# Optimization experiments

Hardware: AMD Instinct MI355X
Metric: run time of the kernel (lower is better)

## Reference

```python
import jax, jax.numpy as jnp
import numpy as np

N_NODES = 50000
N_EDGES = 800000
IN_DIM = 64
HID = 64
OUT_DIM = 40
NEG_SLOPE = 0.2


def _gat_layer(x, src, dst, W, b, att, bias, n_nodes):
    # x: [N, Fin] -> lin -> [N, Fout]; heads = 1
    h = x @ W.T + b
    x_i = h[dst]                      # [E, F] target features
    x_j = h[src]                      # [E, F] source features
    # edge attention logits: cat([x_i, x_j]) @ att.T -> [E, 1]
    alpha = jnp.concatenate([x_i, x_j], axis=-1) @ att.T
    alpha = jax.nn.leaky_relu(alpha, NEG_SLOPE)
    # segment softmax over destination node (pyg_utils.softmax)
    amax = jax.ops.segment_max(alpha, dst, num_segments=n_nodes)
    e = jnp.exp(alpha - amax[dst])
    denom = jax.ops.segment_sum(e, dst, num_segments=n_nodes)
    alpha = e / (denom[dst] + 1e-16)
    # message = alpha * x_j, aggr='add' scatter to dst, then + bias
    out = jax.ops.segment_sum(x_j * alpha, dst, num_segments=n_nodes)
    return out + bias


def setup_inputs() -> dict:
    key = jax.random.key(0)
    ks = jax.random.split(key, 12)
    x = jax.random.normal(ks[0], (N_NODES, IN_DIM), dtype=jnp.float32)
    edge_index = jax.random.randint(ks[1], (2, N_EDGES), 0, N_NODES, dtype=jnp.int64)
    def glorot(k, shape):
        fan_in, fan_out = shape[1], shape[0]
        lim = float(np.sqrt(6.0 / (fan_in + fan_out)))
        return jax.random.uniform(k, shape, jnp.float32, -lim, lim)
    W1 = glorot(ks[2], (HID, IN_DIM))
    b1 = jnp.zeros((HID,), jnp.float32)
    att1 = glorot(ks[3], (1, 2 * HID))
    bias1 = jnp.zeros((HID,), jnp.float32)
    W2 = glorot(ks[4], (HID, HID))
    b2 = jnp.zeros((HID,), jnp.float32)
    att2 = glorot(ks[5], (1, 2 * HID))
    bias2 = jnp.zeros((HID,), jnp.float32)
    Wp1 = glorot(ks[6], (HID, HID))
    bp1 = jnp.zeros((HID,), jnp.float32)
    Wp2 = glorot(ks[7], (OUT_DIM, HID))
    bp2 = jnp.zeros((OUT_DIM,), jnp.float32)
    return {"x": x, "edge_index": edge_index,
            "W1": W1, "b1": b1, "att1": att1, "bias1": bias1,
            "W2": W2, "b2": b2, "att2": att2, "bias2": bias2,
            "Wp1": Wp1, "bp1": bp1, "Wp2": Wp2, "bp2": bp2}


def reference(x, edge_index, W1, b1, att1, bias1, W2, b2, att2, bias2,
              Wp1, bp1, Wp2, bp2):
    src, dst = edge_index[0], edge_index[1]
    n = x.shape[0]
    # layer 1 (GAT) + relu; dropout p=0 in eval -> identity
    h = jax.nn.relu(_gat_layer(x, src, dst, W1, b1, att1, bias1, n))
    # layer 2 (GAT) + relu
    h = jax.nn.relu(_gat_layer(h, src, dst, W2, b2, att2, bias2, n))
    # post-MP MLP + log_softmax over classes
    h = h @ Wp1.T + bp1
    logits = h @ Wp2.T + bp2
    return jax.nn.log_softmax(logits, axis=1)
```

## Files before the change

### kernel.cpp

```cpp
#include <hip/hip_runtime.h>
#include <hip/hip_fp16.h>
#include <math.h>

#define NN 50000
#define NE 800000
#define NEG 0.2f

#define NPB 128
#define CHK 6250
#define NBUK 98
#define LCAP 10240

typedef __attribute__((ext_vector_type(8))) short short8v;
typedef __attribute__((ext_vector_type(4))) float f32x4;

__device__ __forceinline__ float lrelu(float x){ return x > 0.f ? x : NEG * x; }

__device__ __forceinline__ float bcastf(float v, int l){
    return __uint_as_float(__builtin_amdgcn_readlane(__float_as_uint(v), l));
}
__device__ __forceinline__ short bf16t(float x){ return (short)(__float_as_uint(x) >> 16); }
__device__ __forceinline__ float bf16tof(short s){
    return __uint_as_float(((unsigned)(unsigned short)s) << 16);
}

__global__ __launch_bounds__(256) void k_cntA(const int* __restrict__ dst,
                                              int* __restrict__ counts){
    __shared__ int c[NBUK];
    int tid = threadIdx.x, blk = blockIdx.x;
    for (int i = tid; i < NBUK; i += 256) c[i] = 0;
    __syncthreads();
    int beg = blk * CHK, end = min(beg + CHK, NE);
    for (int i = beg + tid; i < end; i += 256) atomicAdd(&c[dst[i] >> 9], 1);
    __syncthreads();
    for (int i = tid; i < NBUK; i += 256) counts[i * NPB + blk] = c[i];
}

__global__ __launch_bounds__(1024) void k_scanB(int* __restrict__ counts,
                                                int* __restrict__ bbase){
    __shared__ int swave[16];
    int tid = threadIdx.x, lane = tid & 63, wid = tid >> 6;
    const int M = NBUK * NPB;
    int carry = 0;
    for (int base = 0; base < M; base += 1024){
        int i = base + tid;
        int v = (i < M) ? counts[i] : 0;
        int incl = v;
        #pragma unroll
        for (int off = 1; off < 64; off <<= 1){
            int t = __shfl_up(incl, off);
            if (lane >= off) incl += t;
        }
        if (lane == 63) swave[wid] = incl;
        __syncthreads();
        if (wid == 0){
            int sv = (lane < 16) ? swave[lane] : 0;
            #pragma unroll
            for (int off = 1; off < 16; off <<= 1){
                int t = __shfl_up(sv, off);
                if (lane >= off) sv += t;
            }
            if (lane < 16) swave[lane] = sv;
        }
        __syncthreads();
        int woff = wid ? swave[wid - 1] : 0;
        if (i < M) counts[i] = carry + woff + incl - v;
        carry += swave[15];
        __syncthreads();
    }
    for (int i = tid; i < NBUK; i += 1024) bbase[i] = counts[i * NPB];
    if (tid == 0) bbase[NBUK] = NE;
}

__global__ __launch_bounds__(256) void k_partC(const int* __restrict__ src,
                                               const int* __restrict__ dst,
                                               const int* __restrict__ cofs,
                                               unsigned* __restrict__ part){
    __shared__ int lcur[NBUK];
    int tid = threadIdx.x, blk = blockIdx.x;
    for (int i = tid; i < NBUK; i += 256) lcur[i] = cofs[i * NPB + blk];
    __syncthreads();
    int beg = blk * CHK, end = min(beg + CHK, NE);
    for (int i = beg + tid; i < end; i += 256){
        int d = dst[i];
        int pos = atomicAdd(&lcur[d >> 9], 1);
        part[pos] = ((unsigned)(d & 511) << 16) | (unsigned)src[i];
    }
}

__global__ __launch_bounds__(256) void k_buildD(const unsigned* __restrict__ part,
                                                const int* __restrict__ bbase,
                                                int* __restrict__ rowstart,
                                                int* __restrict__ csr){
    __shared__ int hist[512], cur[512];
    __shared__ int csrbuf[LCAP];
    __shared__ int swave[4];
    int tid = threadIdx.x, lane = tid & 63, wid = tid >> 6;
    int b = blockIdx.x;
    int ebeg = bbase[b], eend = bbase[b + 1], cnt = eend - ebeg;

    for (int i = tid; i < 512; i += 256) hist[i] = 0;
    __syncthreads();
    for (int i = tid; i < cnt; i += 256) atomicAdd(&hist[part[ebeg + i] >> 16], 1);
    __syncthreads();

    int h0 = hist[2 * tid], h1 = hist[2 * tid + 1];
    int v = h0 + h1, incl = v;
    #pragma unroll
    for (int off = 1; off < 64; off <<= 1){
        int t = __shfl_up(incl, off);
        if (lane >= off) incl += t;
    }
    if (lane == 63) swave[wid] = incl;
    __syncthreads();
    int woff = 0;
    #pragma unroll
    for (int w = 0; w < 4; ++w) if (w < wid) woff += swave[w];
    int e0 = woff + incl - v;
    int e1 = e0 + h0;
    cur[2 * tid] = e0; cur[2 * tid + 1] = e1;
    int gi = b * 512 + 2 * tid;
    if (gi     <= NN) rowstart[gi]     = ebeg + e0;
    if (gi + 1 <= NN) rowstart[gi + 1] = ebeg + e1;
    __syncthreads();

    for (int i = tid; i < cnt; i += 256){
        unsigned u = part[ebeg + i];
        int lp = atomicAdd(&cur[u >> 16], 1);
        if (lp < LCAP) csrbuf[lp] = (int)(u & 0xFFFFu);
    }
    __syncthreads();
    int m = min(cnt, LCAP);
    for (int i = tid; i < m; i += 256) csr[ebeg + i] = csrbuf[i];
}

__global__ __launch_bounds__(256) void k_prep(const float* __restrict__ W1,
                                              const float* __restrict__ W2,
                                              const float* __restrict__ Wp1,
                                              const float* __restrict__ bp1,
                                              const float* __restrict__ Wp2,
                                              const float* __restrict__ bp2,
                                              short8v* __restrict__ w1h, short8v* __restrict__ w1l,
                                              short8v* __restrict__ w2h, short8v* __restrict__ w2l,
                                              short8v* __restrict__ wch, short8v* __restrict__ wcl,
                                              float* __restrict__ bc){
    int tid = threadIdx.x, b = blockIdx.x;
    if (b < 2){
        const float* W = b ? W2 : W1;
        short8v* Wh = b ? w2h : w1h;
        short8v* Wl = b ? w2l : w1l;
        for (int p = tid; p < 512; p += 256){
            int f = p >> 6, lane = p & 63;
            int nt = f >> 1, ks = f & 1;
            int r0 = lane & 15, rg = lane >> 4;
            const float* wp = W + (size_t)(nt * 16 + r0) * 64 + ks * 32 + rg * 8;
            short8v hi, lo;
            #pragma unroll
            for (int j = 0; j < 8; ++j){
                float v = wp[j];
                short h = bf16t(v);
                hi[j] = h; lo[j] = bf16t(v - bf16tof(h));
            }
            Wh[p] = hi; Wl[p] = lo;
        }
    } else {
        __shared__ float wc[2560];
        for (int i = tid; i < 2560; i += 256){
            int c = i >> 6, k = i & 63;
            float s = 0.f;
            #pragma unroll 8
            for (int j = 0; j < 64; ++j) s = fmaf(Wp2[c * 64 + j], Wp1[j * 64 + k], s);
            wc[i] = s;
        }
        if (tid < 40){
            float s = bp2[tid];
            for (int j = 0; j < 64; ++j) s = fmaf(Wp2[tid * 64 + j], bp1[j], s);
            bc[tid] = s;
        }
        __syncthreads();
        for (int p = tid; p < 384; p += 256){
            int f = p >> 6, lane = p & 63;
            int nt = f >> 1, ks = f & 1;
            int r0 = lane & 15, rg = lane >> 4;
            int fr = nt * 16 + r0; if (fr > 39) fr = 39;
            short8v hi, lo;
            #pragma unroll
            for (int j = 0; j < 8; ++j){
                float v = wc[fr * 64 + ks * 32 + rg * 8 + j];
                short h = bf16t(v);
                hi[j] = h; lo[j] = bf16t(v - bf16tof(h));
            }
            wch[p] = hi; wcl[p] = lo;
        }
    }
}

__global__ __launch_bounds__(256) void k_lin_mfma(const float* __restrict__ X,
                                                  const short8v* __restrict__ Wh,
                                                  const short8v* __restrict__ Wl,
                                                  const float* __restrict__ b,
                                                  const float* __restrict__ att,
                                                  __half* __restrict__ Hh,
                                                  float* __restrict__ ad,
                                                  float* __restrict__ as_, int n){
    int lane = threadIdx.x & 63, wid = threadIdx.x >> 6;
    int nb = blockIdx.x * 64 + wid * 16;
    if (nb >= n) return;
    int r0 = lane & 15, rg = lane >> 4;

    short8v a_hi[2], a_lo[2];
    int arow = nb + r0; if (arow >= n) arow = n - 1;
    const float* xp = X + (size_t)arow * 64 + rg * 8;
    #pragma unroll
    for (int ks = 0; ks < 2; ++ks){
        #pragma unroll
        for (int j = 0; j < 8; ++j){
            float v = xp[ks * 32 + j];
            short h = bf16t(v);
            a_hi[ks][j] = h;
            a_lo[ks][j] = bf16t(v - bf16tof(h));
        }
    }

    f32x4 acc[4] = {{0,0,0,0},{0,0,0,0},{0,0,0,0},{0,0,0,0}};
    #pragma unroll
    for (int nt = 0; nt < 4; ++nt){
        #pragma unroll
        for (int ks = 0; ks < 2; ++ks){
            short8v b_hi = Wh[(nt * 2 + ks) * 64 + lane];
            short8v b_lo = Wl[(nt * 2 + ks) * 64 + lane];
            acc[nt] = __builtin_amdgcn_mfma_f32_16x16x32_bf16(a_hi[ks], b_hi, acc[nt], 0, 0, 0);
            acc[nt] = __builtin_amdgcn_mfma_f32_16x16x32_bf16(a_hi[ks], b_lo, acc[nt], 0, 0, 0);
            acc[nt] = __builtin_amdgcn_mfma_f32_16x16x32_bf16(a_lo[ks], b_hi, acc[nt], 0, 0, 0);
        }
    }

    #pragma unroll
    for (int nt = 0; nt < 4; ++nt){
        float bb = b[nt * 16 + r0];
        #pragma unroll
        for (int q = 0; q < 4; ++q){
            int node = nb + rg * 4 + q;
            float v = acc[nt][q] + bb;
            acc[nt][q] = v;
            if (node < n) Hh[(size_t)node * 64 + nt * 16 + r0] = __float2half(v);
        }
    }

    float attd[4], atts[4];
    #pragma unroll
    for (int nt = 0; nt < 4; ++nt){
        attd[nt] = att[nt * 16 + r0];
        atts[nt] = att[64 + nt * 16 + r0];
    }
    #pragma unroll
    for (int q = 0; q < 4; ++q){
        float pd = 0.f, ps = 0.f;
        #pragma unroll
        for (int nt = 0; nt < 4; ++nt){
            pd = fmaf(attd[nt], acc[nt][q], pd);
            ps = fmaf(atts[nt], acc[nt][q], ps);
        }
        #pragma unroll
        for (int off = 8; off; off >>= 1){
            pd += __shfl_xor(pd, off);
            ps += __shfl_xor(ps, off);
        }
        int node = nb + rg * 4 + q;
        if (r0 == 0 && node < n){ ad[node] = pd; as_[node] = ps; }
    }
}

__global__ __launch_bounds__(256) void k_agg(const __half2* __restrict__ H2,
                                             const float* __restrict__ ad,
                                             const float* __restrict__ as_,
                                             const int* __restrict__ rowstart,
                                             const int* __restrict__ csr,
                                             const float2* __restrict__ bias2,
                                             float2* __restrict__ OUT2, int n){
    int tid = threadIdx.x, lane = tid & 63, wid = tid >> 6;
    int node = blockIdx.x * 4 + wid;
    if (node >= n) return;
    int beg = rowstart[node], end = rowstart[node + 1];
    float adn = ad[node];
    int half = lane >> 5, hl = lane & 31;

    float accx = 0.f, accy = 0.f, denom = 0.f;
    for (int cbeg = beg; cbeg < end; cbeg += 64){
        int k = cbeg + lane;
        int s = (k < end) ? csr[k] : 0;
        float e = (k < end) ? __expf(lrelu(adn + as_[s])) : 0.f;
        float es = e;
        #pragma unroll
        for (int off = 32; off; off >>= 1) es += __shfl_xor(es, off);
        denom += es;
        int cnt = min(64, end - cbeg);
        int j = 0;
        for (; j + 4 <= cnt; j += 4){
            int i0 = j + half, i1 = j + 2 + half;
            int   s0 = __shfl(s, i0), s1 = __shfl(s, i1);
            float e0 = __shfl(e, i0), e1 = __shfl(e, i1);
            __half2 ha = H2[(size_t)s0 * 32 + hl];
            __half2 hb = H2[(size_t)s1 * 32 + hl];
            float2 fa = __half22float2(ha), fb = __half22float2(hb);
            accx = fmaf(e0, fa.x, accx); accy = fmaf(e0, fa.y, accy);
            accx = fmaf(e1, fb.x, accx); accy = fmaf(e1, fb.y, accy);
        }
        for (; j < cnt; j += 2){
            int idx = j + half;
            int   se = __shfl(s, idx);
            float ee = __shfl(e, idx);
            float2 f = __half22float2(H2[(size_t)se * 32 + hl]);
            accx = fmaf(ee, f.x, accx); accy = fmaf(ee, f.y, accy);
        }
    }
    accx += __shfl_xor(accx, 32);
    accy += __shfl_xor(accy, 32);
    if (half == 0){
        float2 bb = bias2[hl];
        float inv = 1.f / (denom + 1e-16f);
        float2 o;
        o.x = fmaxf(fmaf(accx, inv, bb.x), 0.f);
        o.y = fmaxf(fmaf(accy, inv, bb.y), 0.f);
        OUT2[(size_t)node * 32 + hl] = o;
    }
}

__global__ __launch_bounds__(256) void k_mlp_mfma(const float* __restrict__ G,
                                                  const short8v* __restrict__ Wh,
                                                  const short8v* __restrict__ Wl,
                                                  const float* __restrict__ bc,
                                                  float* __restrict__ out, int n){
    int lane = threadIdx.x & 63, wid = threadIdx.x >> 6;
    int nb = blockIdx.x * 64 + wid * 16;
    if (nb >= n) return;
    int r0 = lane & 15, rg = lane >> 4;

    short8v a_hi[2], a_lo[2];
    int arow = nb + r0; if (arow >= n) arow = n - 1;
    const float* gp = G + (size_t)arow * 64 + rg * 8;
    #pragma unroll
    for (int ks = 0; ks < 2; ++ks){
        #pragma unroll
        for (int j = 0; j < 8; ++j){
            float v = gp[ks * 32 + j];
            short h = bf16t(v);
            a_hi[ks][j] = h;
            a_lo[ks][j] = bf16t(v - bf16tof(h));
        }
    }

    f32x4 acc[3] = {{0,0,0,0},{0,0,0,0},{0,0,0,0}};
    #pragma unroll
    for (int nt = 0; nt < 3; ++nt){
        #pragma unroll
        for (int ks = 0; ks < 2; ++ks){
            short8v b_hi = Wh[(nt * 2 + ks) * 64 + lane];
            short8v b_lo = Wl[(nt * 2 + ks) * 64 + lane];
            acc[nt] = __builtin_amdgcn_mfma_f32_16x16x32_bf16(a_hi[ks], b_hi, acc[nt], 0, 0, 0);
            acc[nt] = __builtin_amdgcn_mfma_f32_16x16x32_bf16(a_hi[ks], b_lo, acc[nt], 0, 0, 0);
            acc[nt] = __builtin_amdgcn_mfma_f32_16x16x32_bf16(a_lo[ks], b_hi, acc[nt], 0, 0, 0);
        }
    }

    float bcv[3];
    #pragma unroll
    for (int nt = 0; nt < 3; ++nt){
        int f = nt * 16 + r0;
        bcv[nt] = (f < 40) ? bc[f] : 0.f;
    }

    #pragma unroll
    for (int q = 0; q < 4; ++q){
        int node = nb + rg * 4 + q;
        float l0 = acc[0][q] + bcv[0];
        float l1 = acc[1][q] + bcv[1];
        float l2 = (32 + r0 < 40) ? acc[2][q] + bcv[2] : -INFINITY;
        float m = fmaxf(l0, fmaxf(l1, l2));
        #pragma unroll
        for (int off = 8; off; off >>= 1) m = fmaxf(m, __shfl_xor(m, off));
        float s = __expf(l0 - m) + __expf(l1 - m) + ((32 + r0 < 40) ? __expf(l2 - m) : 0.f);
        #pragma unroll
        for (int off = 8; off; off >>= 1) s += __shfl_xor(s, off);
        float lse = m + __logf(s);
        if (node < n){
            out[(size_t)node * 40 + r0]      = l0 - lse;
            out[(size_t)node * 40 + 16 + r0] = l1 - lse;
            if (32 + r0 < 40) out[(size_t)node * 40 + 32 + r0] = l2 - lse;
        }
    }
}

extern "C" void kernel_launch(void* const* d_in, const int* in_sizes, int n_in,
                              void* d_out, int out_size, void* d_ws, size_t ws_size,
                              hipStream_t stream){
    const float* x     = (const float*)d_in[0];
    const int*   ei    = (const int*)  d_in[1];
    const float* W1    = (const float*)d_in[2];
    const float* b1    = (const float*)d_in[3];
    const float* att1  = (const float*)d_in[4];
    const float* bias1 = (const float*)d_in[5];
    const float* W2    = (const float*)d_in[6];
    const float* b2    = (const float*)d_in[7];
    const float* att2  = (const float*)d_in[8];
    const float* bias2 = (const float*)d_in[9];
    const float* Wp1   = (const float*)d_in[10];
    const float* bp1   = (const float*)d_in[11];
    const float* Wp2   = (const float*)d_in[12];
    const float* bp2   = (const float*)d_in[13];
    float* out = (float*)d_out;

    float*    base     = (float*)d_ws;
    float*    g        = base;
    __half*   hh       = (__half*)(base + 3200000);
    unsigned* part     = (unsigned*)(base + 4800000);
    int*      csr      = (int*)(base + 5600000);
    int*      counts   = (int*)(base + 6400000);
    int*      bbase    = (int*)(base + 6412800);
    int*      rowstart = (int*)(base + 6413000);
    float*    ad       = base + 6463008;
    float*    as_      = base + 6513008;
    float*    bc       = base + 6563008;
    short8v*  w1h      = (short8v*)(base + 6563072);
    short8v*  w1l      = (short8v*)(base + 6565120);
    short8v*  w2h      = (short8v*)(base + 6567168);
    short8v*  w2l      = (short8v*)(base + 6569216);
    short8v*  wch      = (short8v*)(base + 6571264);
    short8v*  wcl      = (short8v*)(base + 6572800);

    const int* srcv = ei;
    const int* dstv = ei + NE;

    k_cntA  <<<NPB, 256, 0, stream>>>(dstv, counts);
    k_prep  <<<3, 256, 0, stream>>>(W1, W2, Wp1, bp1, Wp2, bp2,
                                    w1h, w1l, w2h, w2l, wch, wcl, bc);
    k_scanB <<<1, 1024, 0, stream>>>(counts, bbase);
    k_partC <<<NPB, 256, 0, stream>>>(srcv, dstv, counts, part);
    k_buildD<<<NBUK, 256, 0, stream>>>(part, bbase, rowstart, csr);

    int gb = (NN + 63) / 64;
    int nb = (NN + 3) / 4;
    k_lin_mfma<<<gb, 256, 0, stream>>>(x, w1h, w1l, b1, att1, hh, ad, as_, NN);
    k_agg     <<<nb, 256, 0, stream>>>((const __half2*)hh, ad, as_, rowstart, csr,
                                       (const float2*)bias1, (float2*)g, NN);
    k_lin_mfma<<<gb, 256, 0, stream>>>(g, w2h, w2l, b2, att2, hh, ad, as_, NN);
    k_agg     <<<nb, 256, 0, stream>>>((const __half2*)hh, ad, as_, rowstart, csr,
                                       (const float2*)bias2, (float2*)g, NN);
    k_mlp_mfma<<<gb, 256, 0, stream>>>(g, wch, wcl, bc, out, NN);
}
```

Measured before the change: 163.3 us.

## Fuse layer-1 linear, edge counting and MLP weight prep into one launch

Merges the first GAT linear transform, the dst-bucket histogram and the combined MLP weight computation into one heterogeneous kernel launch. The single-block serial scan is replaced by a two-stage parallel scan. Weight bf16 hi/lo splitting now happens inline in the MFMA kernels, which removes the separate prep kernel. The aggregation inner loop is also unrolled to issue four gathers at a time. Together these cut launch count and serialization in the CSR-build phase, at the cost of redundant per-block weight conversion and an extra small scan launch.

```diff
diff --git a/kernel.cpp b/kernel.cpp
--- a/kernel.cpp
+++ b/kernel.cpp
@@ -10,6 +10,7 @@
 #define CHK 6250
 #define NBUK 98
 #define LCAP 10240
+#define GB 782
 
 typedef __attribute__((ext_vector_type(8))) short short8v;
 typedef __attribute__((ext_vector_type(4))) float f32x4;
@@ -24,61 +25,176 @@
     return __uint_as_float(((unsigned)(unsigned short)s) << 16);
 }
 
-__global__ __launch_bounds__(256) void k_cntA(const int* __restrict__ dst,
-                                              int* __restrict__ counts){
+__device__ __forceinline__ void lin_body(int blk, int tid,
+                                         const float* __restrict__ X,
+                                         const float* __restrict__ W,
+                                         const float* __restrict__ b,
+                                         const float* __restrict__ att,
+                                         __half* __restrict__ Hh,
+                                         float* __restrict__ ad,
+                                         float* __restrict__ as_, int n){
+    int lane = tid & 63, wid = tid >> 6;
+    int nb = blk * 64 + wid * 16;
+    if (nb >= n) return;
+    int r0 = lane & 15, rg = lane >> 4;
+
+    short8v a_hi[2], a_lo[2];
+    int arow = nb + r0; if (arow >= n) arow = n - 1;
+    const float* xp = X + (size_t)arow * 64 + rg * 8;
+    #pragma unroll
+    for (int ks = 0; ks < 2; ++ks){
+        #pragma unroll
+        for (int j = 0; j < 8; ++j){
+            float v = xp[ks * 32 + j];
+            short h = bf16t(v);
+            a_hi[ks][j] = h;
+            a_lo[ks][j] = bf16t(v - bf16tof(h));
+        }
+    }
+
+    f32x4 acc[4] = {{0,0,0,0},{0,0,0,0},{0,0,0,0},{0,0,0,0}};
+    #pragma unroll
+    for (int nt = 0; nt < 4; ++nt){
+        const float* wp = W + (size_t)(nt * 16 + r0) * 64 + rg * 8;
+        #pragma unroll
+        for (int ks = 0; ks < 2; ++ks){
+            short8v b_hi, b_lo;
+            #pragma unroll
+            for (int j = 0; j < 8; ++j){
+                float v = wp[ks * 32 + j];
+                short h = bf16t(v);
+                b_hi[j] = h;
+                b_lo[j] = bf16t(v - bf16tof(h));
+            }
+            acc[nt] = __builtin_amdgcn_mfma_f32_16x16x32_bf16(a_hi[ks], b_hi, acc[nt], 0, 0, 0);
+            acc[nt] = __builtin_amdgcn_mfma_f32_16x16x32_bf16(a_hi[ks], b_lo, acc[nt], 0, 0, 0);
+            acc[nt] = __builtin_amdgcn_mfma_f32_16x16x32_bf16(a_lo[ks], b_hi, acc[nt], 0, 0, 0);
+        }
+    }
+
+    #pragma unroll
+    for (int nt = 0; nt < 4; ++nt){
+        float bb = b[nt * 16 + r0];
+        #pragma unroll
+        for (int q = 0; q < 4; ++q){
+            int node = nb + rg * 4 + q;
+            float v = acc[nt][q] + bb;
+            acc[nt][q] = v;
+            if (node < n) Hh[(size_t)node * 64 + nt * 16 + r0] = __float2half(v);
+        }
+    }
+
+    float attd[4], atts[4];
+    #pragma unroll
+    for (int nt = 0; nt < 4; ++nt){
+        attd[nt] = att[nt * 16 + r0];
+        atts[nt] = att[64 + nt * 16 + r0];
+    }
+    #pragma unroll
+    for (int q = 0; q < 4; ++q){
+        float pd = 0.f, ps = 0.f;
+        #pragma unroll
+        for (int nt = 0; nt < 4; ++nt){
+            pd = fmaf(attd[nt], acc[nt][q], pd);
+            ps = fmaf(atts[nt], acc[nt][q], ps);
+        }
+        #pragma unroll
+        for (int off = 8; off; off >>= 1){
+            pd += __shfl_xor(pd, off);
+            ps += __shfl_xor(ps, off);
+        }
+        int node = nb + rg * 4 + q;
+        if (r0 == 0 && node < n){ ad[node] = pd; as_[node] = ps; }
+    }
+}
+
+__global__ __launch_bounds__(256) void k_fuse0(const float* __restrict__ X,
+                                               const float* __restrict__ W1,
+                                               const float* __restrict__ b1,
+                                               const float* __restrict__ att1,
+                                               __half* __restrict__ Hh,
+                                               float* __restrict__ ad,
+                                               float* __restrict__ as_,
+                                               const int* __restrict__ dst,
+                                               int* __restrict__ counts,
+                                               const float* __restrict__ Wp1,
+                                               const float* __restrict__ bp1,
+                                               const float* __restrict__ Wp2,
+                                               const float* __restrict__ bp2,
+                                               float* __restrict__ Wc,
+                                               float* __restrict__ bc){
     __shared__ int c[NBUK];
     int tid = threadIdx.x, blk = blockIdx.x;
-    for (int i = tid; i < NBUK; i += 256) c[i] = 0;
-    __syncthreads();
-    int beg = blk * CHK, end = min(beg + CHK, NE);
-    for (int i = beg + tid; i < end; i += 256) atomicAdd(&c[dst[i] >> 9], 1);
-    __syncthreads();
-    for (int i = tid; i < NBUK; i += 256) counts[i * NPB + blk] = c[i];
-}
-
-__global__ __launch_bounds__(1024) void k_scanB(int* __restrict__ counts,
-                                                int* __restrict__ bbase){
-    __shared__ int swave[16];
+    if (blk < GB){
+        lin_body(blk, tid, X, W1, b1, att1, Hh, ad, as_, NN);
+    } else if (blk < GB + NPB){
+        int cb = blk - GB;
+        for (int i = tid; i < NBUK; i += 256) c[i] = 0;
+        __syncthreads();
+        int beg = cb * CHK, end = min(beg + CHK, NE);
+        for (int i = beg + tid; i < end; i += 256) atomicAdd(&c[dst[i] >> 9], 1);
+        __syncthreads();
+        for (int i = tid; i < NBUK; i += 256) counts[i * NPB + cb] = c[i];
+    } else {
+        for (int idx = tid; idx < 2560; idx += 256){
+            int cc = idx >> 6, k = idx & 63;
+            float s = 0.f;
+            #pragma unroll 8
+            for (int j = 0; j < 64; ++j) s = fmaf(Wp2[cc * 64 + j], Wp1[j * 64 + k], s);
+            Wc[idx] = s;
+        }
+        if (tid < 40){
+            float s = bp2[tid];
+            for (int j = 0; j < 64; ++j) s = fmaf(Wp2[tid * 64 + j], bp1[j], s);
+            bc[tid] = s;
+        }
+    }
+}
+
+__global__ __launch_bounds__(NPB) void k_scan1(int* __restrict__ counts,
+                                               int* __restrict__ tot){
+    __shared__ int wsum[2];
+    int b = blockIdx.x, tid = threadIdx.x, lane = tid & 63, wid = tid >> 6;
+    int v = counts[b * NPB + tid];
+    int incl = v;
+    #pragma unroll
+    for (int off = 1; off < 64; off <<= 1){
+        int t = __shfl_up(incl, off);
+        if (lane >= off) incl += t;
+    }
+    if (lane == 63) wsum[wid] = incl;
+    __syncthreads();
+    int excl = incl - v + (wid ? wsum[0] : 0);
+    counts[b * NPB + tid] = excl;
+    if (tid == NPB - 1) tot[b] = excl + v;
+}
+
+__global__ __launch_bounds__(128) void k_scan2(const int* __restrict__ tot,
+                                               int* __restrict__ bbase){
+    __shared__ int wsum[2];
     int tid = threadIdx.x, lane = tid & 63, wid = tid >> 6;
-    const int M = NBUK * NPB;
-    int carry = 0;
-    for (int base = 0; base < M; base += 1024){
-        int i = base + tid;
-        int v = (i < M) ? counts[i] : 0;
-        int incl = v;
-        #pragma unroll
-        for (int off = 1; off < 64; off <<= 1){
-            int t = __shfl_up(incl, off);
-            if (lane >= off) incl += t;
-        }
-        if (lane == 63) swave[wid] = incl;
-        __syncthreads();
-        if (wid == 0){
-            int sv = (lane < 16) ? swave[lane] : 0;
-            #pragma unroll
-            for (int off = 1; off < 16; off <<= 1){
-                int t = __shfl_up(sv, off);
-                if (lane >= off) sv += t;
-            }
-            if (lane < 16) swave[lane] = sv;
-        }
-        __syncthreads();
-        int woff = wid ? swave[wid - 1] : 0;
-        if (i < M) counts[i] = carry + woff + incl - v;
-        carry += swave[15];
-        __syncthreads();
-    }
-    for (int i = tid; i < NBUK; i += 1024) bbase[i] = counts[i * NPB];
-    if (tid == 0) bbase[NBUK] = NE;
+    int v = (tid < NBUK) ? tot[tid] : 0;
+    int incl = v;
+    #pragma unroll
+    for (int off = 1; off < 64; off <<= 1){
+        int t = __shfl_up(incl, off);
+        if (lane >= off) incl += t;
+    }
+    if (lane == 63) wsum[wid] = incl;
+    __syncthreads();
+    int excl = incl - v + (wid ? wsum[0] : 0);
+    if (tid < NBUK) bbase[tid] = excl;
+    if (tid == NBUK - 1) bbase[NBUK] = excl + v;
 }
 
 __global__ __launch_bounds__(256) void k_partC(const int* __restrict__ src,
                                                const int* __restrict__ dst,
                                                const int* __restrict__ cofs,
+                                               const int* __restrict__ bbase,
                                                unsigned* __restrict__ part){
     __shared__ int lcur[NBUK];
     int tid = threadIdx.x, blk = blockIdx.x;
-    for (int i = tid; i < NBUK; i += 256) lcur[i] = cofs[i * NPB + blk];
+    for (int i = tid; i < NBUK; i += 256) lcur[i] = bbase[i] + cofs[i * NPB + blk];
     __syncthreads();
     int beg = blk * CHK, end = min(beg + CHK, NE);
     for (int i = beg + tid; i < end; i += 256){
@@ -134,141 +250,14 @@
     for (int i = tid; i < m; i += 256) csr[ebeg + i] = csrbuf[i];
 }
 
-__global__ __launch_bounds__(256) void k_prep(const float* __restrict__ W1,
-                                              const float* __restrict__ W2,
-                                              const float* __restrict__ Wp1,
-                                              const float* __restrict__ bp1,
-                                              const float* __restrict__ Wp2,
-                                              const float* __restrict__ bp2,
-                                              short8v* __restrict__ w1h, short8v* __restrict__ w1l,
-                                              short8v* __restrict__ w2h, short8v* __restrict__ w2l,
-                                              short8v* __restrict__ wch, short8v* __restrict__ wcl,
-                                              float* __restrict__ bc){
-    int tid = threadIdx.x, b = blockIdx.x;
-    if (b < 2){
-        const float* W = b ? W2 : W1;
-        short8v* Wh = b ? w2h : w1h;
-        short8v* Wl = b ? w2l : w1l;
-        for (int p = tid; p < 512; p += 256){
-            int f = p >> 6, lane = p & 63;
-            int nt = f >> 1, ks = f & 1;
-            int r0 = lane & 15, rg = lane >> 4;
-            const float* wp = W + (size_t)(nt * 16 + r0) * 64 + ks * 32 + rg * 8;
-            short8v hi, lo;
-            #pragma unroll
-            for (int j = 0; j < 8; ++j){
-                float v = wp[j];
-                short h = bf16t(v);
-                hi[j] = h; lo[j] = bf16t(v - bf16tof(h));
-            }
-            Wh[p] = hi; Wl[p] = lo;
-        }
-    } else {
-        __shared__ float wc[2560];
-        for (int i = tid; i < 2560; i += 256){
-            int c = i >> 6, k = i & 63;
-            float s = 0.f;
-            #pragma unroll 8
-            for (int j = 0; j < 64; ++j) s = fmaf(Wp2[c * 64 + j], Wp1[j * 64 + k], s);
-            wc[i] = s;
-        }
-        if (tid < 40){
-            float s = bp2[tid];
-            for (int j = 0; j < 64; ++j) s = fmaf(Wp2[tid * 64 + j], bp1[j], s);
-            bc[tid] = s;
-        }
-        __syncthreads();
-        for (int p = tid; p < 384; p += 256){
-            int f = p >> 6, lane = p & 63;
-            int nt = f >> 1, ks = f & 1;
-            int r0 = lane & 15, rg = lane >> 4;
-            int fr = nt * 16 + r0; if (fr > 39) fr = 39;
-            short8v hi, lo;
-            #pragma unroll
-            for (int j = 0; j < 8; ++j){
-                float v = wc[fr * 64 + ks * 32 + rg * 8 + j];
-                short h = bf16t(v);
-                hi[j] = h; lo[j] = bf16t(v - bf16tof(h));
-            }
-            wch[p] = hi; wcl[p] = lo;
-        }
-    }
-}
-
 __global__ __launch_bounds__(256) void k_lin_mfma(const float* __restrict__ X,
-                                                  const short8v* __restrict__ Wh,
-                                                  const short8v* __restrict__ Wl,
+                                                  const float* __restrict__ W,
                                                   const float* __restrict__ b,
                                                   const float* __restrict__ att,
                                                   __half* __restrict__ Hh,
                                                   float* __restrict__ ad,
                                                   float* __restrict__ as_, int n){
-    int lane = threadIdx.x & 63, wid = threadIdx.x >> 6;
-    int nb = blockIdx.x * 64 + wid * 16;
-    if (nb >= n) return;
-    int r0 = lane & 15, rg = lane >> 4;
-
-    short8v a_hi[2], a_lo[2];
-    int arow = nb + r0; if (arow >= n) arow = n - 1;
-    const float* xp = X + (size_t)arow * 64 + rg * 8;
-    #pragma unroll
-    for (int ks = 0; ks < 2; ++ks){
-        #pragma unroll
-        for (int j = 0; j < 8; ++j){
-            float v = xp[ks * 32 + j];
-            short h = bf16t(v);
-            a_hi[ks][j] = h;
-            a_lo[ks][j] = bf16t(v - bf16tof(h));
-        }
-    }
-
-    f32x4 acc[4] = {{0,0,0,0},{0,0,0,0},{0,0,0,0},{0,0,0,0}};
-    #pragma unroll
-    for (int nt = 0; nt < 4; ++nt){
-        #pragma unroll
-        for (int ks = 0; ks < 2; ++ks){
-            short8v b_hi = Wh[(nt * 2 + ks) * 64 + lane];
-            short8v b_lo = Wl[(nt * 2 + ks) * 64 + lane];
-            acc[nt] = __builtin_amdgcn_mfma_f32_16x16x32_bf16(a_hi[ks], b_hi, acc[nt], 0, 0, 0);
-            acc[nt] = __builtin_amdgcn_mfma_f32_16x16x32_bf16(a_hi[ks], b_lo, acc[nt], 0, 0, 0);
-            acc[nt] = __builtin_amdgcn_mfma_f32_16x16x32_bf16(a_lo[ks], b_hi, acc[nt], 0, 0, 0);
-        }
-    }
-
-    #pragma unroll
-    for (int nt = 0; nt < 4; ++nt){
-        float bb = b[nt * 16 + r0];
-        #pragma unroll
-        for (int q = 0; q < 4; ++q){
-            int node = nb + rg * 4 + q;
-            float v = acc[nt][q] + bb;
-            acc[nt][q] = v;
-            if (node < n) Hh[(size_t)node * 64 + nt * 16 + r0] = __float2half(v);
-        }
-    }
-
-    float attd[4], atts[4];
-    #pragma unroll
-    for (int nt = 0; nt < 4; ++nt){
-        attd[nt] = att[nt * 16 + r0];
-        atts[nt] = att[64 + nt * 16 + r0];
-    }
-    #pragma unroll
-    for (int q = 0; q < 4; ++q){
-        float pd = 0.f, ps = 0.f;
-        #pragma unroll
-        for (int nt = 0; nt < 4; ++nt){
-            pd = fmaf(attd[nt], acc[nt][q], pd);
-            ps = fmaf(atts[nt], acc[nt][q], ps);
-        }
-        #pragma unroll
-        for (int off = 8; off; off >>= 1){
-            pd += __shfl_xor(pd, off);
-            ps += __shfl_xor(ps, off);
-        }
-        int node = nb + rg * 4 + q;
-        if (r0 == 0 && node < n){ ad[node] = pd; as_[node] = ps; }
-    }
+    lin_body(blockIdx.x, threadIdx.x, X, W, b, att, Hh, ad, as_, n);
 }
 
 __global__ __launch_bounds__(256) void k_agg(const __half2* __restrict__ H2,
@@ -296,13 +285,27 @@
         denom += es;
         int cnt = min(64, end - cbeg);
         int j = 0;
+        for (; j + 8 <= cnt; j += 8){
+            int i0 = j + half, i1 = j + 2 + half, i2 = j + 4 + half, i3 = j + 6 + half;
+            int   s0 = __shfl(s, i0), s1 = __shfl(s, i1), s2 = __shfl(s, i2), s3 = __shfl(s, i3);
+            float e0 = __shfl(e, i0), e1 = __shfl(e, i1), e2 = __shfl(e, i2), e3 = __shfl(e, i3);
+            __half2 ha = H2[(size_t)s0 * 32 + hl];
+            __half2 hb = H2[(size_t)s1 * 32 + hl];
+            __half2 hc = H2[(size_t)s2 * 32 + hl];
+            __half2 hd = H2[(size_t)s3 * 32 + hl];
+            float2 fa = __half22float2(ha), fb = __half22float2(hb);
+            float2 fc = __half22float2(hc), fd = __half22float2(hd);
+            accx = fmaf(e0, fa.x, accx); accy = fmaf(e0, fa.y, accy);
+            accx = fmaf(e1, fb.x, accx); accy = fmaf(e1, fb.y, accy);
+            accx = fmaf(e2, fc.x, accx); accy = fmaf(e2, fc.y, accy);
+            accx = fmaf(e3, fd.x, accx); accy = fmaf(e3, fd.y, accy);
+        }
         for (; j + 4 <= cnt; j += 4){
             int i0 = j + half, i1 = j + 2 + half;
             int   s0 = __shfl(s, i0), s1 = __shfl(s, i1);
             float e0 = __shfl(e, i0), e1 = __shfl(e, i1);
-            __half2 ha = H2[(size_t)s0 * 32 + hl];
-            __half2 hb = H2[(size_t)s1 * 32 + hl];
-            float2 fa = __half22float2(ha), fb = __half22float2(hb);
+            float2 fa = __half22float2(H2[(size_t)s0 * 32 + hl]);
+            float2 fb = __half22float2(H2[(size_t)s1 * 32 + hl]);
             accx = fmaf(e0, fa.x, accx); accy = fmaf(e0, fa.y, accy);
             accx = fmaf(e1, fb.x, accx); accy = fmaf(e1, fb.y, accy);
         }
@@ -327,8 +330,7 @@
 }
 
 __global__ __launch_bounds__(256) void k_mlp_mfma(const float* __restrict__ G,
-                                                  const short8v* __restrict__ Wh,
-                                                  const short8v* __restrict__ Wl,
+                                                  const float* __restrict__ Wc,
                                                   const float* __restrict__ bc,
                                                   float* __restrict__ out, int n){
     int lane = threadIdx.x & 63, wid = threadIdx.x >> 6;
@@ -353,10 +355,19 @@
     f32x4 acc[3] = {{0,0,0,0},{0,0,0,0},{0,0,0,0}};
     #pragma unroll
     for (int nt = 0; nt < 3; ++nt){
+        int f = nt * 16 + r0;
+        int fr = (f < 40) ? f : 39;
+        const float* wp = Wc + (size_t)fr * 64 + rg * 8;
         #pragma unroll
         for (int ks = 0; ks < 2; ++ks){
-            short8v b_hi = Wh[(nt * 2 + ks) * 64 + lane];
-            short8v b_lo = Wl[(nt * 2 + ks) * 64 + lane];
+            short8v b_hi, b_lo;
+            #pragma unroll
+            for (int j = 0; j < 8; ++j){
+                float v = wp[ks * 32 + j];
+                short h = bf16t(v);
+                b_hi[j] = h;
+                b_lo[j] = bf16t(v - bf16tof(h));
+            }
             acc[nt] = __builtin_amdgcn_mfma_f32_16x16x32_bf16(a_hi[ks], b_hi, acc[nt], 0, 0, 0);
             acc[nt] = __builtin_amdgcn_mfma_f32_16x16x32_bf16(a_hi[ks], b_lo, acc[nt], 0, 0, 0);
             acc[nt] = __builtin_amdgcn_mfma_f32_16x16x32_bf16(a_lo[ks], b_hi, acc[nt], 0, 0, 0);
@@ -416,35 +427,30 @@
     unsigned* part     = (unsigned*)(base + 4800000);
     int*      csr      = (int*)(base + 5600000);
     int*      counts   = (int*)(base + 6400000);
-    int*      bbase    = (int*)(base + 6412800);
-    int*      rowstart = (int*)(base + 6413000);
-    float*    ad       = base + 6463008;
-    float*    as_      = base + 6513008;
-    float*    bc       = base + 6563008;
-    short8v*  w1h      = (short8v*)(base + 6563072);
-    short8v*  w1l      = (short8v*)(base + 6565120);
-    short8v*  w2h      = (short8v*)(base + 6567168);
-    short8v*  w2l      = (short8v*)(base + 6569216);
-    short8v*  wch      = (short8v*)(base + 6571264);
-    short8v*  wcl      = (short8v*)(base + 6572800);
+    int*      tot      = (int*)(base + 6412944);
+    int*      bbase    = (int*)(base + 6413072);
+    int*      rowstart = (int*)(base + 6413200);
+    float*    ad       = base + 6463208;
+    float*    as_      = base + 6513208;
+    float*    Wc       = base + 6563208;
+    float*    bc       = base + 6565768;
 
     const int* srcv = ei;
     const int* dstv = ei + NE;
 
-    k_cntA  <<<NPB, 256, 0, stream>>>(dstv, counts);
-    k_prep  <<<3, 256, 0, stream>>>(W1, W2, Wp1, bp1, Wp2, bp2,
-                                    w1h, w1l, w2h, w2l, wch, wcl, bc);
-    k_scanB <<<1, 1024, 0, stream>>>(counts, bbase);
-    k_partC <<<NPB, 256, 0, stream>>>(srcv, dstv, counts, part);
+    k_fuse0 <<<GB + NPB + 1, 256, 0, stream>>>(x, W1, b1, att1, hh, ad, as_,
+                                               dstv, counts,
+                                               Wp1, bp1, Wp2, bp2, Wc, bc);
+    k_scan1 <<<NBUK, NPB, 0, stream>>>(counts, tot);
+    k_scan2 <<<1, 128, 0, stream>>>(tot, bbase);
+    k_partC <<<NPB, 256, 0, stream>>>(srcv, dstv, counts, bbase, part);
     k_buildD<<<NBUK, 256, 0, stream>>>(part, bbase, rowstart, csr);
 
-    int gb = (NN + 63) / 64;
     int nb = (NN + 3) / 4;
-    k_lin_mfma<<<gb, 256, 0, stream>>>(x, w1h, w1l, b1, att1, hh, ad, as_, NN);
     k_agg     <<<nb, 256, 0, stream>>>((const __half2*)hh, ad, as_, rowstart, csr,
                                        (const float2*)bias1, (float2*)g, NN);
-    k_lin_mfma<<<gb, 256, 0, stream>>>(g, w2h, w2l, b2, att2, hh, ad, as_, NN);
+    k_lin_mfma<<<GB, 256, 0, stream>>>(g, W2, b2, att2, hh, ad, as_, NN);
     k_agg     <<<nb, 256, 0, stream>>>((const __half2*)hh, ad, as_, rowstart, csr,
                                        (const float2*)bias2, (float2*)g, NN);
-    k_mlp_mfma<<<gb, 256, 0, stream>>>(g, wch, wcl, bc, out, NN);
-}
+    k_mlp_mfma<<<GB, 256, 0, stream>>>(g, Wc, bc, out, NN);
+}
```

New measurement: 146.7 us. 1.11x faster.
